# Performance work log

Measured on AMD Instinct MI355X. Metric: run time of the kernel, lower is better.

## Reference

```python
import jax, jax.numpy as jnp
import numpy as np

EPS = 1e-12  # undefined global `eps` in the original source; standard tiny epsilon


def setup_inputs() -> dict:
    key = jax.random.key(0)
    k1, k2 = jax.random.split(key)
    B, C = 32768, 1000
    output = jax.random.normal(k1, (B, C), dtype=jnp.float32)
    multilabels = (jax.random.uniform(k2, (B, C)) < 0.05).astype(jnp.float32)
    multilabels = multilabels.at[:, 0].set(1.0)
    return {"output": output, "multilabels": multilabels}


def reference(output, multilabels):
    # Equivalent closed form of: for every nonempty subset g of true labels,
    #   loss(g) = -[ pseudo_y*log(o+eps) + (1-pseudo_y)*log(1-o+eps) ].sum()
    #           = base - sum_{j in g} gain_j,
    # with base = -sum_j log(1-o_j+eps) and gain_j = log(o_j+eps)-log(1-o_j+eps).
    # min over nonempty subsets = base - max nonempty-subset gain
    #   = base - (sum of positive gains over true labels, or the max single
    #      gain among true labels if all gains are negative).
    o = jax.nn.sigmoid(output)                      # [B, C]
    log_p = jnp.log(o + EPS)
    log_np = jnp.log(1.0 - o + EPS)
    base = -jnp.sum(log_np, axis=1)                 # [B]
    gain = log_p - log_np                           # [B, C]
    is_true = multilabels == 1.0                    # [B, C] bool (constant)
    pos = is_true & (gain > 0)
    pos_gain = jnp.sum(jnp.where(pos, gain, 0.0), axis=1)          # [B]
    any_pos = jnp.any(pos, axis=1)                                  # [B]
    best_single = jnp.max(jnp.where(is_true, gain, -jnp.inf), axis=1)  # [B]
    max_gain = jnp.where(any_pos, pos_gain, best_single)
    per_sample = base - max_gain                    # [B]
    return jnp.mean(per_sample)
```

## Files before the change

### kernel.cpp

```cpp
#include <hip/hip_runtime.h>
#include <math.h>


constexpr int B = 32768;
constexpr int C = 1000;
constexpr int C4 = C / 4;
constexpr int BLOCKS = 2048;
constexpr int THREADS = 256;
constexpr int WAVES_PER_BLOCK = THREADS / 64;
constexpr int TOTAL_WAVES = BLOCKS * WAVES_PER_BLOCK;
constexpr int TAIL_LANES = C4 - 192;

__device__ __forceinline__ void elem_update(float x, float m,
                                            float& base, float& pos, float& best) {
    float e  = __expf(-fabsf(x));
    float xp = fmaxf(x, 0.0f);
    base += xp + __logf(1.0f + e);
    pos  += m * xp;
    if (m != 0.0f) best = fmaxf(best, x);
}

__device__ __forceinline__ void vec_update(float4 x, float4 m,
                                           float& base, float& pos, float& best) {
    elem_update(x.x, m.x, base, pos, best);
    elem_update(x.y, m.y, base, pos, best);
    elem_update(x.z, m.z, base, pos, best);
    elem_update(x.w, m.w, base, pos, best);
}

__global__ __launch_bounds__(THREADS)
void row_loss_kernel(const float* __restrict__ X,
                     const float* __restrict__ M,
                     float* __restrict__ partial) {
    const int wave_in_block = threadIdx.x >> 6;
    const int lane          = threadIdx.x & 63;
    const int gwave         = blockIdx.x * WAVES_PER_BLOCK + wave_in_block;

    float acc = 0.0f;

    for (int row = gwave; row < B; row += TOTAL_WAVES) {
        const float4* x4 = reinterpret_cast<const float4*>(X + (size_t)row * C);
        const float4* m4 = reinterpret_cast<const float4*>(M + (size_t)row * C);

        float4 xa = x4[lane];
        float4 xb = x4[lane + 64];
        float4 xc = x4[lane + 128];
        float4 ma = m4[lane];
        float4 mb = m4[lane + 64];
        float4 mc = m4[lane + 128];
        float4 xd = make_float4(-INFINITY, -INFINITY, -INFINITY, -INFINITY);
        float4 md = make_float4(0.0f, 0.0f, 0.0f, 0.0f);
        if (lane < TAIL_LANES) {
            xd = x4[lane + 192];
            md = m4[lane + 192];
        }

        float b0 = 0.f, b1 = 0.f, b2 = 0.f, b3 = 0.f;
        float p0 = 0.f, p1 = 0.f, p2 = 0.f, p3 = 0.f;
        float s0 = -INFINITY, s1 = -INFINITY, s2 = -INFINITY, s3 = -INFINITY;

        vec_update(xa, ma, b0, p0, s0);
        vec_update(xb, mb, b1, p1, s1);
        vec_update(xc, mc, b2, p2, s2);
        vec_update(xd, md, b3, p3, s3);

        float base = (b0 + b1) + (b2 + b3);
        float pos  = (p0 + p1) + (p2 + p3);
        float best = fmaxf(fmaxf(s0, s1), fmaxf(s2, s3));

        #pragma unroll
        for (int off = 32; off > 0; off >>= 1) {
            base += __shfl_down(base, off, 64);
            pos  += __shfl_down(pos,  off, 64);
            best  = fmaxf(best, __shfl_down(best, off, 64));
        }

        if (lane == 0) {
            float max_gain = (pos > 0.0f) ? pos : best;
            acc += base - max_gain;
        }
    }

    __shared__ float s[WAVES_PER_BLOCK];
    if (lane == 0) s[wave_in_block] = acc;
    __syncthreads();
    if (threadIdx.x == 0) {
        float t = 0.0f;
        #pragma unroll
        for (int i = 0; i < WAVES_PER_BLOCK; ++i) t += s[i];
        partial[blockIdx.x] = t;
    }
}

__global__ __launch_bounds__(256)
void finalize_kernel(const float* __restrict__ partial, float* __restrict__ out) {
    double t = 0.0;
    for (int i = threadIdx.x; i < BLOCKS; i += 256) t += (double)partial[i];

    #pragma unroll
    for (int off = 32; off > 0; off >>= 1)
        t += __shfl_down(t, off, 64);

    __shared__ double s[4];
    const int lane = threadIdx.x & 63;
    const int w    = threadIdx.x >> 6;
    if (lane == 0) s[w] = t;
    __syncthreads();
    if (threadIdx.x == 0) {
        double r = s[0] + s[1] + s[2] + s[3];
        out[0] = (float)(r / (double)B);
    }
}

extern "C" void kernel_launch(void* const* d_in, const int* in_sizes, int n_in,
                              void* d_out, int out_size, void* d_ws, size_t ws_size,
                              hipStream_t stream) {
    const float* X   = (const float*)d_in[0];
    const float* M   = (const float*)d_in[1];
    float* out       = (float*)d_out;
    float* partial   = (float*)d_ws;

    row_loss_kernel<<<BLOCKS, THREADS, 0, stream>>>(X, M, partial);
    finalize_kernel<<<1, 256, 0, stream>>>(partial, out);
}
```

Baseline: 271.8 us.

## Map four rows per wave with 16-lane groups and staged register prefetch

Each wave now handles four rows at once, with one 16-lane group per row, replacing the grid-stride loop that processed one row per wave. Loads are issued in staged batches so the next chunk is already in flight while the current one is computed. The aim is more outstanding memory requests per wave, to hide latency on this bandwidth-bound reduction. The cost is higher register use and a row mapping tied to the fixed grid size.

```diff
diff --git a/kernel.cpp b/kernel.cpp
--- a/kernel.cpp
+++ b/kernel.cpp
@@ -4,12 +4,9 @@
 
 constexpr int B = 32768;
 constexpr int C = 1000;
-constexpr int C4 = C / 4;
 constexpr int BLOCKS = 2048;
 constexpr int THREADS = 256;
-constexpr int WAVES_PER_BLOCK = THREADS / 64;
-constexpr int TOTAL_WAVES = BLOCKS * WAVES_PER_BLOCK;
-constexpr int TAIL_LANES = C4 - 192;
+constexpr int WAVES_PER_BLOCK = 4;
 
 __device__ __forceinline__ void elem_update(float x, float m,
                                             float& base, float& pos, float& best) {
@@ -20,7 +17,7 @@
     if (m != 0.0f) best = fmaxf(best, x);
 }
 
-__device__ __forceinline__ void vec_update(float4 x, float4 m,
+__device__ __forceinline__ void vec_update(const float4& x, const float4& m,
                                            float& base, float& pos, float& best) {
     elem_update(x.x, m.x, base, pos, best);
     elem_update(x.y, m.y, base, pos, best);
@@ -32,57 +29,61 @@
 void row_loss_kernel(const float* __restrict__ X,
                      const float* __restrict__ M,
                      float* __restrict__ partial) {
+    const int lane = threadIdx.x & 63;
+    const int sub  = lane & 15;
+    const int grp  = lane >> 4;
     const int wave_in_block = threadIdx.x >> 6;
-    const int lane          = threadIdx.x & 63;
-    const int gwave         = blockIdx.x * WAVES_PER_BLOCK + wave_in_block;
+    const int gwave = blockIdx.x * WAVES_PER_BLOCK + wave_in_block;
+    const int row   = gwave * 4 + grp;
 
-    float acc = 0.0f;
+    const float4* x4 = reinterpret_cast<const float4*>(X + (size_t)row * C);
+    const float4* m4 = reinterpret_cast<const float4*>(M + (size_t)row * C);
 
-    for (int row = gwave; row < B; row += TOTAL_WAVES) {
-        const float4* x4 = reinterpret_cast<const float4*>(X + (size_t)row * C);
-        const float4* m4 = reinterpret_cast<const float4*>(M + (size_t)row * C);
+    float4 xA[4], mA[4], xB[4], mB[4];
 
-        float4 xa = x4[lane];
-        float4 xb = x4[lane + 64];
-        float4 xc = x4[lane + 128];
-        float4 ma = m4[lane];
-        float4 mb = m4[lane + 64];
-        float4 mc = m4[lane + 128];
-        float4 xd = make_float4(-INFINITY, -INFINITY, -INFINITY, -INFINITY);
-        float4 md = make_float4(0.0f, 0.0f, 0.0f, 0.0f);
-        if (lane < TAIL_LANES) {
-            xd = x4[lane + 192];
-            md = m4[lane + 192];
-        }
+    #pragma unroll
+    for (int j = 0; j < 4; ++j) { int i = sub + 16*j;       xA[j] = x4[i]; mA[j] = m4[i]; }
+    #pragma unroll
+    for (int j = 0; j < 4; ++j) { int i = sub + 64 + 16*j;  xB[j] = x4[i]; mB[j] = m4[i]; }
 
-        float b0 = 0.f, b1 = 0.f, b2 = 0.f, b3 = 0.f;
-        float p0 = 0.f, p1 = 0.f, p2 = 0.f, p3 = 0.f;
-        float s0 = -INFINITY, s1 = -INFINITY, s2 = -INFINITY, s3 = -INFINITY;
+    float base = 0.f, pos = 0.f, best = -INFINITY;
 
-        vec_update(xa, ma, b0, p0, s0);
-        vec_update(xb, mb, b1, p1, s1);
-        vec_update(xc, mc, b2, p2, s2);
-        vec_update(xd, md, b3, p3, s3);
+    #pragma unroll
+    for (int j = 0; j < 4; ++j) vec_update(xA[j], mA[j], base, pos, best);
 
-        float base = (b0 + b1) + (b2 + b3);
-        float pos  = (p0 + p1) + (p2 + p3);
-        float best = fmaxf(fmaxf(s0, s1), fmaxf(s2, s3));
+    #pragma unroll
+    for (int j = 0; j < 4; ++j) { int i = sub + 128 + 16*j; xA[j] = x4[i]; mA[j] = m4[i]; }
 
-        #pragma unroll
-        for (int off = 32; off > 0; off >>= 1) {
-            base += __shfl_down(base, off, 64);
-            pos  += __shfl_down(pos,  off, 64);
-            best  = fmaxf(best, __shfl_down(best, off, 64));
-        }
+    #pragma unroll
+    for (int j = 0; j < 4; ++j) vec_update(xB[j], mB[j], base, pos, best);
 
-        if (lane == 0) {
-            float max_gain = (pos > 0.0f) ? pos : best;
-            acc += base - max_gain;
-        }
+    #pragma unroll
+    for (int j = 0; j < 3; ++j) { int i = sub + 192 + 16*j; xB[j] = x4[i]; mB[j] = m4[i]; }
+    if (sub < 10) { xB[3] = x4[sub + 240]; mB[3] = m4[sub + 240]; }
+    else {
+        xB[3] = make_float4(-1e30f, -1e30f, -1e30f, -1e30f);
+        mB[3] = make_float4(0.f, 0.f, 0.f, 0.f);
     }
 
+    #pragma unroll
+    for (int j = 0; j < 4; ++j) vec_update(xA[j], mA[j], base, pos, best);
+    #pragma unroll
+    for (int j = 0; j < 4; ++j) vec_update(xB[j], mB[j], base, pos, best);
+
+    #pragma unroll
+    for (int off = 8; off > 0; off >>= 1) {
+        base += __shfl_down(base, off, 16);
+        pos  += __shfl_down(pos,  off, 16);
+        best  = fmaxf(best, __shfl_down(best, off, 16));
+    }
+
+    float per = base - ((pos > 0.f) ? pos : best);
+    float v = (sub == 0) ? per : 0.f;
+    v += __shfl_down(v, 32, 64);
+    v += __shfl_down(v, 16, 64);
+
     __shared__ float s[WAVES_PER_BLOCK];
-    if (lane == 0) s[wave_in_block] = acc;
+    if (lane == 0) s[wave_in_block] = v;
     __syncthreads();
     if (threadIdx.x == 0) {
         float t = 0.0f;
@@ -115,10 +116,10 @@
 extern "C" void kernel_launch(void* const* d_in, const int* in_sizes, int n_in,
                               void* d_out, int out_size, void* d_ws, size_t ws_size,
                               hipStream_t stream) {
-    const float* X   = (const float*)d_in[0];
-    const float* M   = (const float*)d_in[1];
-    float* out       = (float*)d_out;
-    float* partial   = (float*)d_ws;
+    const float* X  = (const float*)d_in[0];
+    const float* M  = (const float*)d_in[1];
+    float* out      = (float*)d_out;
+    float* partial  = (float*)d_ws;
 
     row_loss_kernel<<<BLOCKS, THREADS, 0, stream>>>(X, M, partial);
     finalize_kernel<<<1, 256, 0, stream>>>(partial, out);
```

Result: no change. 274.3 us (+0.9%).
